# Kernel tuning notes

Hardware: AMD Instinct MI355X
Metric: run time of the kernel (lower is better)

## Reference

```python
import jax, jax.numpy as jnp
import numpy as np

Q, G, H, K, C, O = 20000, 20000, 32, 15, 128, 128


def setup_inputs() -> dict:
    key = jax.random.key(0)
    k1, k2, k3, k4, k5, k6 = jax.random.split(key, 6)
    return {
        "query_points": jax.random.normal(k1, (Q, 3), dtype=jnp.float32),
        "support_points": jax.random.normal(k2, (G, 3), dtype=jnp.float32),
        "support_features": jax.random.normal(k3, (G, C), dtype=jnp.float32),
        "kernel": jax.random.normal(k4, (K, 3), dtype=jnp.float32),
        "weights": jax.random.normal(k5, (K, C, O), dtype=jnp.float32),
        # KDTree KNN indices are precomputed int constants; random in-range
        # indices give identical math/perf characteristics.
        "neighbor_indices": jax.random.randint(k6, (Q, H), 0, G, dtype=jnp.int32),
    }


def reference(query_points, support_points, support_features, kernel, weights, neighbor_indices):
    # Faithful to original: neighbor_points gathered from query_points
    # (original code indexes query_points, not support_points; requires Q == G).
    neighbor_points = query_points[neighbor_indices]          # [Q, H, 3]
    neighbor_features = support_features[neighbor_indices]    # [Q, H, C]
    # diff: [Q, H, K, 3] = neighbor - query - kernel_point
    diff = neighbor_points[:, :, None, :] - query_points[:, None, None, :] - kernel
    distances = jnp.sqrt(jnp.sum(diff * diff, axis=-1))        # [Q, H, K]
    sigma = 1.0
    influences = jax.nn.relu(1.0 - distances / sigma)          # [Q, H, K]
    # 3-way contraction over h, k, c  -> [Q, O]
    result = jnp.einsum("qhk,kco,qhc->qo", influences, weights, neighbor_features)
    return result
```

## Files before the change

kernel.cpp:

```cpp
#include <hip/hip_runtime.h>


typedef short bf16x8 __attribute__((ext_vector_type(8)));
typedef float f32x4 __attribute__((ext_vector_type(4)));

constexpr int Qn = 20000;
constexpr int Hn = 32;
constexpr int Kn = 15;
constexpr int Cn = 128;
constexpr int On = 128;
constexpr int QB = 16;
constexpr int ROWS = Kn * Cn;
constexpr int KT = ROWS / 32;
constexpr int NT = On / 16;
constexpr int BLOCK = 256;

constexpr int F_OFF    = 0;
constexpr int INFL_OFF = 61440;
constexpr int NIDX_OFF = INFL_OFF + 16384;
constexpr int QP_OFF   = NIDX_OFF + 2048;
constexpr int KP_OFF   = QP_OFF + 256;
constexpr int FLG_OFF  = KP_OFF + 256;
constexpr int POOL_SZ  = FLG_OFF + 64;

__device__ __forceinline__ unsigned short f2bf(float x) {
  unsigned u = __float_as_uint(x);
  unsigned r = u + 0x7fffu + ((u >> 16) & 1u);
  return (unsigned short)(r >> 16);
}
__device__ __forceinline__ float bflo(unsigned u) { return __uint_as_float(u << 16); }
__device__ __forceinline__ float bfhi(unsigned u) { return __uint_as_float(u & 0xffff0000u); }

__global__ void conv_w(const float* __restrict__ wts, unsigned short* __restrict__ wfrag) {
  int tid = blockIdx.x * 256 + threadIdx.x;
  if (tid >= KT * NT * 64) return;
  int l = tid & 63, nt = (tid >> 6) & 7, kt = tid >> 9;
  int col = nt * 16 + (l & 15);
  int r0 = kt * 32 + (l >> 4) * 8;
  unsigned short v[8];
#pragma unroll
  for (int j = 0; j < 8; ++j) v[j] = f2bf(wts[(r0 + j) * On + col]);
  uint4 o;
  o.x = (unsigned)v[0] | ((unsigned)v[1] << 16);
  o.y = (unsigned)v[2] | ((unsigned)v[3] << 16);
  o.z = (unsigned)v[4] | ((unsigned)v[5] << 16);
  o.w = (unsigned)v[6] | ((unsigned)v[7] << 16);
  *(uint4*)(wfrag + (size_t)tid * 8) = o;
}

__global__ __launch_bounds__(BLOCK, 2)
void kpconv_main(const float* __restrict__ qpts,
                 const float* __restrict__ sfeat,
                 const float* __restrict__ kpts,
                 const int* __restrict__ nidx,
                 const unsigned short* __restrict__ wfrag,
                 float* __restrict__ out) {
  __shared__ __align__(16) char pool[POOL_SZ];
  unsigned short* infl = (unsigned short*)(pool + INFL_OFF);
  int*      nidxl = (int*)(pool + NIDX_OFF);
  float*    qpl   = (float*)(pool + QP_OFF);
  float*    kpl   = (float*)(pool + KP_OFF);
  unsigned* flg   = (unsigned*)(pool + FLG_OFF);
  float*    npt   = (float*)pool;

  const int t = threadIdx.x;
  const int qbase = blockIdx.x * QB;

  if (t < 16) {
    flg[t] = 0;
    qpl[t * 4 + 0] = qpts[(qbase + t) * 3 + 0];
    qpl[t * 4 + 1] = qpts[(qbase + t) * 3 + 1];
    qpl[t * 4 + 2] = qpts[(qbase + t) * 3 + 2];
  } else if (t >= 16 && t < 16 + Kn) {
    int k = t - 16;
    kpl[k * 4 + 0] = kpts[k * 3 + 0];
    kpl[k * 4 + 1] = kpts[k * 3 + 1];
    kpl[k * 4 + 2] = kpts[k * 3 + 2];
  }
  for (int idx = t; idx < QB * Hn; idx += BLOCK) {
    int g = nidx[(size_t)qbase * Hn + idx];
    nidxl[idx] = g;
    npt[idx * 4 + 0] = qpts[g * 3 + 0];
    npt[idx * 4 + 1] = qpts[g * 3 + 1];
    npt[idx * 4 + 2] = qpts[g * 3 + 2];
  }
  __syncthreads();

  for (int idx = t; idx < QB * Hn * 16; idx += BLOCK) {
    int k = idx & 15, h = (idx >> 4) & 31, q = idx >> 9;
    unsigned short v = 0;
    if (k < Kn) {
      float dx = npt[(q * 32 + h) * 4 + 0] - qpl[q * 4 + 0] - kpl[k * 4 + 0];
      float dy = npt[(q * 32 + h) * 4 + 1] - qpl[q * 4 + 1] - kpl[k * 4 + 1];
      float dz = npt[(q * 32 + h) * 4 + 2] - qpl[q * 4 + 2] - kpl[k * 4 + 2];
      float d = sqrtf(dx * dx + dy * dy + dz * dz);
      float inf = fmaxf(0.f, 1.f - d);
      if (inf > 0.f) atomicOr(&flg[q], 1u << h);
      v = f2bf(inf);
    }
    infl[idx] = v;
  }
  __syncthreads();

  {
    const int c = t & 127;
    const int qh = t >> 7;
    for (int i = 0; i < 8; ++i) {
      const int q = qh * 8 + i;
      unsigned m = flg[q];
      float facc[15];
#pragma unroll
      for (int k = 0; k < 15; ++k) facc[k] = 0.f;
      while (m) {
        int h = __ffs(m) - 1; m &= m - 1;
        int g = nidxl[q * 32 + h];
        float feat = sfeat[(size_t)g * Cn + c];
        const uint4* ip = (const uint4*)(infl + (q * 32 + h) * 16);
        uint4 A = ip[0], B = ip[1];
        facc[0]  += bflo(A.x) * feat; facc[1]  += bfhi(A.x) * feat;
        facc[2]  += bflo(A.y) * feat; facc[3]  += bfhi(A.y) * feat;
        facc[4]  += bflo(A.z) * feat; facc[5]  += bfhi(A.z) * feat;
        facc[6]  += bflo(A.w) * feat; facc[7]  += bfhi(A.w) * feat;
        facc[8]  += bflo(B.x) * feat; facc[9]  += bfhi(B.x) * feat;
        facc[10] += bflo(B.y) * feat; facc[11] += bfhi(B.y) * feat;
        facc[12] += bflo(B.z) * feat; facc[13] += bfhi(B.z) * feat;
        facc[14] += bflo(B.w) * feat;
      }
      const unsigned rb = (unsigned)q * (ROWS * 2);
      const unsigned sw = ((unsigned)q & 7u) << 4;
#pragma unroll
      for (int k = 0; k < 15; ++k) {
        unsigned byte = (rb + (unsigned)(k * Cn + c) * 2u) ^ sw;
        *(unsigned short*)(pool + byte) = f2bf(facc[k]);
      }
    }
  }
  __syncthreads();

  {
    const int l = t & 63, w = t >> 6;
    const int nt0 = w * 2, nt1 = nt0 + 1;
    const int arow = l & 15;
    const unsigned kgoff = (unsigned)(l >> 4) * 16u;
    const unsigned abase = (unsigned)arow * (ROWS * 2);
    const unsigned aswz = ((unsigned)arow & 7u) << 4;
    const uint4* wf = (const uint4*)wfrag;

    f32x4 acc0 = {0.f, 0.f, 0.f, 0.f}, acc1 = {0.f, 0.f, 0.f, 0.f};
    bf16x8 aA, aB; uint4 b0A, b1A, b0B, b1B;

#define LOADA(kt) { aA = *(const bf16x8*)(pool + ((abase + (unsigned)(kt) * 64u + kgoff) ^ aswz)); \
                    b0A = wf[((kt) * NT + nt0) * 64 + l]; b1A = wf[((kt) * NT + nt1) * 64 + l]; }
#define LOADB(kt) { aB = *(const bf16x8*)(pool + ((abase + (unsigned)(kt) * 64u + kgoff) ^ aswz)); \
                    b0B = wf[((kt) * NT + nt0) * 64 + l]; b1B = wf[((kt) * NT + nt1) * 64 + l]; }

    LOADA(0); LOADB(1);
#pragma unroll
    for (int kt = 0; kt < KT; kt += 2) {
      { bf16x8 bb0 = *(bf16x8*)&b0A, bb1 = *(bf16x8*)&b1A;
        acc0 = __builtin_amdgcn_mfma_f32_16x16x32_bf16(aA, bb0, acc0, 0, 0, 0);
        acc1 = __builtin_amdgcn_mfma_f32_16x16x32_bf16(aA, bb1, acc1, 0, 0, 0); }
      if (kt + 2 < KT) LOADA(kt + 2);
      { bf16x8 bb0 = *(bf16x8*)&b0B, bb1 = *(bf16x8*)&b1B;
        acc0 = __builtin_amdgcn_mfma_f32_16x16x32_bf16(aB, bb0, acc0, 0, 0, 0);
        acc1 = __builtin_amdgcn_mfma_f32_16x16x32_bf16(aB, bb1, acc1, 0, 0, 0); }
      if (kt + 3 < KT) LOADB(kt + 3);
    }
#undef LOADA
#undef LOADB

    const int orow = (l >> 4) * 4;
    const int ocol = l & 15;
    float* obase = out + (size_t)qbase * On;
#pragma unroll
    for (int r = 0; r < 4; ++r) {
      obase[(orow + r) * On + nt0 * 16 + ocol] = acc0[r];
      obase[(orow + r) * On + nt1 * 16 + ocol] = acc1[r];
    }
  }
}

extern "C" void kernel_launch(void* const* d_in, const int* in_sizes, int n_in,
                              void* d_out, int out_size, void* d_ws, size_t ws_size,
                              hipStream_t stream) {
  const float* qpts  = (const float*)d_in[0];
  const float* sfeat = (const float*)d_in[2];
  const float* kpts  = (const float*)d_in[3];
  const float* wts   = (const float*)d_in[4];
  const int*   nidx  = (const int*)d_in[5];
  float* outp = (float*)d_out;
  unsigned short* wfrag = (unsigned short*)d_ws;

  conv_w<<<(KT * NT * 64 + 255) / 256, 256, 0, stream>>>(wts, wfrag);
  kpconv_main<<<Qn / QB, BLOCK, 0, stream>>>(qpts, sfeat, kpts, nidx, wfrag, outp);
}
```

Measured before the change: 228.0 us.

## Compute per-query influence-feature contraction with MFMA over compacted neighbor lists

Replaces the scalar per-thread FMA loop that built the [q, k*c] intermediate with a per-query MFMA that multiplies the compacted influence matrix (k by active neighbors) by gathered bf16 features. Active neighbors are compacted into per-query lists, and the intermediate is laid out as c*16+k padded to 2048 columns, with the weight fragments repacked to match. The block grows to 512 threads at one block per CU, and the second GEMM now gives each wave one output tile with two accumulators. This trades scalar FMA work for matrix-core work, at the cost of extra bf16 rounding of features and partial sums, padded K, and lower occupancy.

New measurement: 190.3 us. 1.2x faster.

```diff
diff --git a/kernel.cpp b/kernel.cpp
--- a/kernel.cpp
+++ b/kernel.cpp
@@ -10,36 +10,43 @@
 constexpr int Cn = 128;
 constexpr int On = 128;
 constexpr int QB = 16;
-constexpr int ROWS = Kn * Cn;
-constexpr int KT = ROWS / 32;
+constexpr int CK = 2048;
+constexpr int KT = CK / 32;
 constexpr int NT = On / 16;
-constexpr int BLOCK = 256;
-
-constexpr int F_OFF    = 0;
-constexpr int INFL_OFF = 61440;
-constexpr int NIDX_OFF = INFL_OFF + 16384;
-constexpr int QP_OFF   = NIDX_OFF + 2048;
-constexpr int KP_OFF   = QP_OFF + 256;
-constexpr int FLG_OFF  = KP_OFF + 256;
-constexpr int POOL_SZ  = FLG_OFF + 64;
+constexpr int BLOCK = 512;
+
+constexpr int F_OFF     = 0;
+constexpr int NPT_OFF   = 0;
+constexpr int DENSE_OFF = 8192;
+constexpr int INFL_OFF  = 65536;
+constexpr int GLIST_OFF = 81920;
+constexpr int NIDX_OFF  = 83968;
+constexpr int HLIST_OFF = 86016;
+constexpr int CNT_OFF   = 87040;
+constexpr int QPL_OFF   = 87104;
+constexpr int KPL_OFF   = 87360;
+constexpr int FLG_OFF   = 87616;
+constexpr int POOL_SZ   = 87680;
 
 __device__ __forceinline__ unsigned short f2bf(float x) {
   unsigned u = __float_as_uint(x);
   unsigned r = u + 0x7fffu + ((u >> 16) & 1u);
   return (unsigned short)(r >> 16);
 }
-__device__ __forceinline__ float bflo(unsigned u) { return __uint_as_float(u << 16); }
-__device__ __forceinline__ float bfhi(unsigned u) { return __uint_as_float(u & 0xffff0000u); }
 
 __global__ void conv_w(const float* __restrict__ wts, unsigned short* __restrict__ wfrag) {
   int tid = blockIdx.x * 256 + threadIdx.x;
   if (tid >= KT * NT * 64) return;
   int l = tid & 63, nt = (tid >> 6) & 7, kt = tid >> 9;
   int col = nt * 16 + (l & 15);
-  int r0 = kt * 32 + (l >> 4) * 8;
+  int ck0 = kt * 32 + (l >> 4) * 8;
   unsigned short v[8];
 #pragma unroll
-  for (int j = 0; j < 8; ++j) v[j] = f2bf(wts[(r0 + j) * On + col]);
+  for (int j = 0; j < 8; ++j) {
+    int ck = ck0 + j;
+    int k = ck & 15, c = ck >> 4;
+    v[j] = (k < Kn) ? f2bf(wts[(k * Cn + c) * On + col]) : (unsigned short)0;
+  }
   uint4 o;
   o.x = (unsigned)v[0] | ((unsigned)v[1] << 16);
   o.y = (unsigned)v[2] | ((unsigned)v[3] << 16);
@@ -48,7 +55,7 @@
   *(uint4*)(wfrag + (size_t)tid * 8) = o;
 }
 
-__global__ __launch_bounds__(BLOCK, 2)
+__global__ __launch_bounds__(BLOCK, 1)
 void kpconv_main(const float* __restrict__ qpts,
                  const float* __restrict__ sfeat,
                  const float* __restrict__ kpts,
@@ -56,127 +63,142 @@
                  const unsigned short* __restrict__ wfrag,
                  float* __restrict__ out) {
   __shared__ __align__(16) char pool[POOL_SZ];
-  unsigned short* infl = (unsigned short*)(pool + INFL_OFF);
-  int*      nidxl = (int*)(pool + NIDX_OFF);
-  float*    qpl   = (float*)(pool + QP_OFF);
-  float*    kpl   = (float*)(pool + KP_OFF);
-  unsigned* flg   = (unsigned*)(pool + FLG_OFF);
-  float*    npt   = (float*)pool;
-
   const int t = threadIdx.x;
   const int qbase = blockIdx.x * QB;
-
-  if (t < 16) {
-    flg[t] = 0;
-    qpl[t * 4 + 0] = qpts[(qbase + t) * 3 + 0];
-    qpl[t * 4 + 1] = qpts[(qbase + t) * 3 + 1];
-    qpl[t * 4 + 2] = qpts[(qbase + t) * 3 + 2];
-  } else if (t >= 16 && t < 16 + Kn) {
-    int k = t - 16;
-    kpl[k * 4 + 0] = kpts[k * 3 + 0];
-    kpl[k * 4 + 1] = kpts[k * 3 + 1];
-    kpl[k * 4 + 2] = kpts[k * 3 + 2];
-  }
-  for (int idx = t; idx < QB * Hn; idx += BLOCK) {
-    int g = nidx[(size_t)qbase * Hn + idx];
-    nidxl[idx] = g;
-    npt[idx * 4 + 0] = qpts[g * 3 + 0];
-    npt[idx * 4 + 1] = qpts[g * 3 + 1];
-    npt[idx * 4 + 2] = qpts[g * 3 + 2];
-  }
-  __syncthreads();
-
-  for (int idx = t; idx < QB * Hn * 16; idx += BLOCK) {
+  const int l = t & 63, w = t >> 6;
+  const int lg = l >> 4, li = l & 15;
+
+  {
+    int g = nidx[(size_t)qbase * Hn + t];
+    *(int*)(pool + NIDX_OFF + t * 4) = g;
+    float* np = (float*)(pool + NPT_OFF + t * 16);
+    np[0] = qpts[g * 3 + 0];
+    np[1] = qpts[g * 3 + 1];
+    np[2] = qpts[g * 3 + 2];
+    uint4 z = {0, 0, 0, 0};
+    *(uint4*)(pool + INFL_OFF + t * 32) = z;
+    *(uint4*)(pool + INFL_OFF + t * 32 + 16) = z;
+    if (t < 16) {
+      *(unsigned*)(pool + FLG_OFF + t * 4) = 0u;
+      float* qp = (float*)(pool + QPL_OFF + t * 16);
+      qp[0] = qpts[(qbase + t) * 3 + 0];
+      qp[1] = qpts[(qbase + t) * 3 + 1];
+      qp[2] = qpts[(qbase + t) * 3 + 2];
+    }
+    if (t >= 32 && t < 32 + Kn) {
+      int k = t - 32;
+      float* kp = (float*)(pool + KPL_OFF + k * 16);
+      kp[0] = kpts[k * 3 + 0];
+      kp[1] = kpts[k * 3 + 1];
+      kp[2] = kpts[k * 3 + 2];
+    }
+  }
+  __syncthreads();
+
+#pragma unroll
+  for (int it = 0; it < 16; ++it) {
+    int idx = t + it * BLOCK;
     int k = idx & 15, h = (idx >> 4) & 31, q = idx >> 9;
     unsigned short v = 0;
     if (k < Kn) {
-      float dx = npt[(q * 32 + h) * 4 + 0] - qpl[q * 4 + 0] - kpl[k * 4 + 0];
-      float dy = npt[(q * 32 + h) * 4 + 1] - qpl[q * 4 + 1] - kpl[k * 4 + 1];
-      float dz = npt[(q * 32 + h) * 4 + 2] - qpl[q * 4 + 2] - kpl[k * 4 + 2];
+      const float* np = (const float*)(pool + NPT_OFF + (q * 32 + h) * 16);
+      const float* qp = (const float*)(pool + QPL_OFF + q * 16);
+      const float* kp = (const float*)(pool + KPL_OFF + k * 16);
+      float dx = np[0] - qp[0] - kp[0];
+      float dy = np[1] - qp[1] - kp[1];
+      float dz = np[2] - qp[2] - kp[2];
       float d = sqrtf(dx * dx + dy * dy + dz * dz);
       float inf = fmaxf(0.f, 1.f - d);
-      if (inf > 0.f) atomicOr(&flg[q], 1u << h);
+      if (inf > 0.f) atomicOr((unsigned*)(pool + FLG_OFF) + q, 1u << h);
       v = f2bf(inf);
     }
-    infl[idx] = v;
+    *(unsigned short*)(pool + DENSE_OFF + q * 1024 + h * 32 + k * 2) = v;
+  }
+  __syncthreads();
+
+  if (t < 16) {
+    unsigned m = *(unsigned*)(pool + FLG_OFF + t * 4);
+    int cnt = __popc(m);
+    *(int*)(pool + CNT_OFF + t * 4) = cnt;
+    int i = 0;
+    while (m) {
+      int h = __ffs(m) - 1; m &= m - 1;
+      *(short*)(pool + HLIST_OFF + t * 64 + i * 2) = (short)h;
+      *(int*)(pool + GLIST_OFF + t * 128 + i * 4) = *(int*)(pool + NIDX_OFF + (t * 32 + h) * 4);
+      ++i;
+    }
+  }
+  __syncthreads();
+
+#pragma unroll
+  for (int it = 0; it < 16; ++it) {
+    int idx = t + it * BLOCK;
+    int slot = idx & 31, k = (idx >> 5) & 15, q = idx >> 9;
+    int cnt = *(const int*)(pool + CNT_OFF + q * 4);
+    if (k < Kn && slot < cnt) {
+      int h = *(const short*)(pool + HLIST_OFF + q * 64 + slot * 2);
+      unsigned short v = *(const unsigned short*)(pool + DENSE_OFF + q * 1024 + h * 32 + k * 2);
+      unsigned byte = (unsigned)(q * 1024) + (((unsigned)(k * 64 + slot * 2)) ^ (((unsigned)k & 7u) << 4));
+      *(unsigned short*)(pool + INFL_OFF + byte) = v;
+    }
   }
   __syncthreads();
 
   {
-    const int c = t & 127;
-    const int qh = t >> 7;
-    for (int i = 0; i < 8; ++i) {
-      const int q = qh * 8 + i;
-      unsigned m = flg[q];
-      float facc[15];
-#pragma unroll
-      for (int k = 0; k < 15; ++k) facc[k] = 0.f;
-      while (m) {
-        int h = __ffs(m) - 1; m &= m - 1;
-        int g = nidxl[q * 32 + h];
-        float feat = sfeat[(size_t)g * Cn + c];
-        const uint4* ip = (const uint4*)(infl + (q * 32 + h) * 16);
-        uint4 A = ip[0], B = ip[1];
-        facc[0]  += bflo(A.x) * feat; facc[1]  += bfhi(A.x) * feat;
-        facc[2]  += bflo(A.y) * feat; facc[3]  += bfhi(A.y) * feat;
-        facc[4]  += bflo(A.z) * feat; facc[5]  += bfhi(A.z) * feat;
-        facc[6]  += bflo(A.w) * feat; facc[7]  += bfhi(A.w) * feat;
-        facc[8]  += bflo(B.x) * feat; facc[9]  += bfhi(B.x) * feat;
-        facc[10] += bflo(B.y) * feat; facc[11] += bfhi(B.y) * feat;
-        facc[12] += bflo(B.z) * feat; facc[13] += bfhi(B.z) * feat;
-        facc[14] += bflo(B.w) * feat;
-      }
-      const unsigned rb = (unsigned)q * (ROWS * 2);
-      const unsigned sw = ((unsigned)q & 7u) << 4;
-#pragma unroll
-      for (int k = 0; k < 15; ++k) {
-        unsigned byte = (rb + (unsigned)(k * Cn + c) * 2u) ^ sw;
-        *(unsigned short*)(pool + byte) = f2bf(facc[k]);
-      }
+    const unsigned abase0 = (unsigned)INFL_OFF +
+        (((unsigned)(li * 64 + lg * 16)) ^ (((unsigned)li & 7u) << 4));
+    const int cbase = w * 16 + li;
+    for (int q = 0; q < QB; ++q) {
+      bf16x8 afrag = *(const bf16x8*)(pool + abase0 + q * 1024);
+      uint4 ga = *(const uint4*)(pool + GLIST_OFF + q * 128 + lg * 32);
+      uint4 gb = *(const uint4*)(pool + GLIST_OFF + q * 128 + lg * 32 + 16);
+      int cnt = *(const int*)(pool + CNT_OFF + q * 4);
+      int s0 = lg * 8;
+      float v0 = (s0 + 0 < cnt) ? sfeat[(size_t)ga.x * Cn + cbase] : 0.f;
+      float v1 = (s0 + 1 < cnt) ? sfeat[(size_t)ga.y * Cn + cbase] : 0.f;
+      float v2 = (s0 + 2 < cnt) ? sfeat[(size_t)ga.z * Cn + cbase] : 0.f;
+      float v3 = (s0 + 3 < cnt) ? sfeat[(size_t)ga.w * Cn + cbase] : 0.f;
+      float v4 = (s0 + 4 < cnt) ? sfeat[(size_t)gb.x * Cn + cbase] : 0.f;
+      float v5 = (s0 + 5 < cnt) ? sfeat[(size_t)gb.y * Cn + cbase] : 0.f;
+      float v6 = (s0 + 6 < cnt) ? sfeat[(size_t)gb.z * Cn + cbase] : 0.f;
+      float v7 = (s0 + 7 < cnt) ? sfeat[(size_t)gb.w * Cn + cbase] : 0.f;
+      uint4 bu;
+      bu.x = (unsigned)f2bf(v0) | ((unsigned)f2bf(v1) << 16);
+      bu.y = (unsigned)f2bf(v2) | ((unsigned)f2bf(v3) << 16);
+      bu.z = (unsigned)f2bf(v4) | ((unsigned)f2bf(v5) << 16);
+      bu.w = (unsigned)f2bf(v6) | ((unsigned)f2bf(v7) << 16);
+      bf16x8 bfrag = *(bf16x8*)&bu;
+      f32x4 zero = {0.f, 0.f, 0.f, 0.f};
+      f32x4 d = __builtin_amdgcn_mfma_f32_16x16x32_bf16(afrag, bfrag, zero, 0, 0, 0);
+      unsigned wb = ((unsigned)(cbase * 32 + lg * 8) ^ (((unsigned)q & 7u) << 4)) + (unsigned)(q * 4096);
+      uint2 pk;
+      pk.x = (unsigned)f2bf(d[0]) | ((unsigned)f2bf(d[1]) << 16);
+      pk.y = (unsigned)f2bf(d[2]) | ((unsigned)f2bf(d[3]) << 16);
+      *(uint2*)(pool + F_OFF + wb) = pk;
     }
   }
   __syncthreads();
 
   {
-    const int l = t & 63, w = t >> 6;
-    const int nt0 = w * 2, nt1 = nt0 + 1;
-    const int arow = l & 15;
-    const unsigned kgoff = (unsigned)(l >> 4) * 16u;
-    const unsigned abase = (unsigned)arow * (ROWS * 2);
-    const unsigned aswz = ((unsigned)arow & 7u) << 4;
-    const uint4* wf = (const uint4*)wfrag;
-
+    const int nt = w;
+    const unsigned fb = (unsigned)(li * 4096 + lg * 16);
+    const unsigned fswz = ((unsigned)li & 7u) << 4;
+    const uint4* wf = (const uint4*)wfrag + (size_t)nt * 64 + l;
     f32x4 acc0 = {0.f, 0.f, 0.f, 0.f}, acc1 = {0.f, 0.f, 0.f, 0.f};
-    bf16x8 aA, aB; uint4 b0A, b1A, b0B, b1B;
-
-#define LOADA(kt) { aA = *(const bf16x8*)(pool + ((abase + (unsigned)(kt) * 64u + kgoff) ^ aswz)); \
-                    b0A = wf[((kt) * NT + nt0) * 64 + l]; b1A = wf[((kt) * NT + nt1) * 64 + l]; }
-#define LOADB(kt) { aB = *(const bf16x8*)(pool + ((abase + (unsigned)(kt) * 64u + kgoff) ^ aswz)); \
-                    b0B = wf[((kt) * NT + nt0) * 64 + l]; b1B = wf[((kt) * NT + nt1) * 64 + l]; }
-
-    LOADA(0); LOADB(1);
-#pragma unroll
+#pragma unroll 8
     for (int kt = 0; kt < KT; kt += 2) {
-      { bf16x8 bb0 = *(bf16x8*)&b0A, bb1 = *(bf16x8*)&b1A;
-        acc0 = __builtin_amdgcn_mfma_f32_16x16x32_bf16(aA, bb0, acc0, 0, 0, 0);
-        acc1 = __builtin_amdgcn_mfma_f32_16x16x32_bf16(aA, bb1, acc1, 0, 0, 0); }
-      if (kt + 2 < KT) LOADA(kt + 2);
-      { bf16x8 bb0 = *(bf16x8*)&b0B, bb1 = *(bf16x8*)&b1B;
-        acc0 = __builtin_amdgcn_mfma_f32_16x16x32_bf16(aB, bb0, acc0, 0, 0, 0);
-        acc1 = __builtin_amdgcn_mfma_f32_16x16x32_bf16(aB, bb1, acc1, 0, 0, 0); }
-      if (kt + 3 < KT) LOADB(kt + 3);
-    }
-#undef LOADA
-#undef LOADB
-
-    const int orow = (l >> 4) * 4;
-    const int ocol = l & 15;
+      bf16x8 a0 = *(const bf16x8*)(pool + F_OFF + ((fb + (unsigned)(kt * 64)) ^ fswz));
+      uint4 w0 = wf[(size_t)kt * 512];
+      bf16x8 a1 = *(const bf16x8*)(pool + F_OFF + ((fb + (unsigned)(kt * 64 + 64)) ^ fswz));
+      uint4 w1 = wf[(size_t)kt * 512 + 512];
+      acc0 = __builtin_amdgcn_mfma_f32_16x16x32_bf16(a0, *(bf16x8*)&w0, acc0, 0, 0, 0);
+      acc1 = __builtin_amdgcn_mfma_f32_16x16x32_bf16(a1, *(bf16x8*)&w1, acc1, 0, 0, 0);
+    }
+    f32x4 acc = acc0 + acc1;
     float* obase = out + (size_t)qbase * On;
 #pragma unroll
-    for (int r = 0; r < 4; ++r) {
-      obase[(orow + r) * On + nt0 * 16 + ocol] = acc0[r];
-      obase[(orow + r) * On + nt1 * 16 + ocol] = acc1[r];
-    }
+    for (int r = 0; r < 4; ++r)
+      obase[(lg * 4 + r) * On + nt * 16 + li] = acc[r];
   }
 }
 
```
